# Optimization experiments

Hardware: AMD Instinct MI355X
Metric: run time of the kernel (lower is better)

Reference implementation:

```python
import math
import jax, jax.numpy as jnp
import numpy as np

B, T, D = 2, 1024, 512
H, DK = 8, 64


def setup_inputs() -> dict:
    key = jax.random.key(0)
    ks = jax.random.split(key, 7)
    s = 1.0 / math.sqrt(D)
    x = jax.random.normal(ks[0], (B, T, D), dtype=jnp.float32)
    Wq = jax.random.normal(ks[1], (D, H * DK), dtype=jnp.float32) * s
    Wk = jax.random.normal(ks[2], (D, H * DK), dtype=jnp.float32) * s
    Wv = jax.random.normal(ks[3], (D, H * DK), dtype=jnp.float32) * s
    Wo = jax.random.normal(ks[4], (H * DK, D), dtype=jnp.float32) * s
    Wg = jax.random.normal(ks[5], (D, H * DK), dtype=jnp.float32) * 0.02
    bg = jnp.ones((H * DK,), dtype=jnp.float32)  # gate_bias_init = 1.0
    return {"x": x, "Wq": Wq, "Wk": Wk, "Wv": Wv, "Wo": Wo, "Wg": Wg, "bg": bg}


def reference(x, Wq, Wk, Wv, Wo, Wg, bg):
    b, t, d = x.shape
    Q = jax.nn.relu(x @ Wq).reshape(b, t, H, DK)
    K = jax.nn.relu(x @ Wk).reshape(b, t, H, DK)
    V = (x @ Wv).reshape(b, t, H, DK)
    angle = jnp.arange(t, dtype=x.dtype) * (math.pi / (2 * t))  # (T,)
    cosw = jnp.cos(angle)[None, :, None, None]
    sinw = jnp.sin(angle)[None, :, None, None]
    Qc, Qs = Q * cosw, Q * sinw
    Kc, Ks = K * cosw, K * sinw
    # cumulative KV outer products: (B,T,H,DK,DK)
    Sc = jnp.cumsum(jnp.einsum('bthd,bthe->bthde', Kc, V), axis=1)
    Ss = jnp.cumsum(jnp.einsum('bthd,bthe->bthde', Ks, V), axis=1)
    o = jnp.einsum('bthd,bthde->bthe', Qc, Sc) + jnp.einsum('bthd,bthde->bthe', Qs, Ss)
    zc = jnp.cumsum(Kc, axis=1)
    zs = jnp.cumsum(Ks, axis=1)
    z = jnp.einsum('bthd,bthd->bth', Qc, zc) + jnp.einsum('bthd,bthd->bth', Qs, zs)
    z = jnp.maximum(z, 1e-6)[..., None]
    o = o / z
    gate = jax.nn.sigmoid((x @ Wg + bg).reshape(b, t, H, DK))
    o = o * gate
    return o.reshape(b, t, H * DK) @ Wo
```

## Files before the change

kernel.cpp:

```cpp
#include <hip/hip_runtime.h>
#include <math.h>

#define B_ 2
#define T_ 1024
#define D_ 512
#define H_ 8
#define DK_ 64
#define NBH_ 16
#define C_ 32
#define G_ 32

#define PI_OVER_2T 0.00153398078788564122971808758949f

typedef float f32x4 __attribute__((ext_vector_type(4)));
typedef short s16x8 __attribute__((ext_vector_type(8)));

__device__ __forceinline__ ushort f2bf(float x) {
    unsigned u = __float_as_uint(x);
    unsigned r = (u + 0x7fffu + ((u >> 16) & 1u)) >> 16;
    return (ushort)r;
}
__device__ __forceinline__ float bf2f(ushort u) {
    return __uint_as_float((unsigned)u << 16);
}

__device__ __forceinline__ void async16(void* lds, const void* g) {
    __builtin_amdgcn_global_load_lds(
        (const __attribute__((address_space(1))) void*)g,
        (__attribute__((address_space(3))) void*)lds, 16, 0, 0);
}

__global__ __launch_bounds__(256) void k_conv(
    const float* __restrict__ x,
    const float* __restrict__ Wq, const float* __restrict__ Wk,
    const float* __restrict__ Wv, const float* __restrict__ Wg,
    const float* __restrict__ Wo,
    ushort* __restrict__ xb, ushort* __restrict__ WtAll)
{
    __shared__ float Ts[64][65];
    const int bx = blockIdx.x;
    const int tid = threadIdx.x;
    if (bx < 1024) {
        int i = (bx * 256 + tid) * 4;
        float4 v = *(const float4*)&x[i];
        ushort4 o;
        o.x = f2bf(v.x); o.y = f2bf(v.y); o.z = f2bf(v.z); o.w = f2bf(v.w);
        *(ushort4*)&xb[i] = o;
        return;
    }
    const int bid = bx - 1024;
    const int mi = bid >> 6;
    const int t64 = bid & 63;
    const float* __restrict__ W = (mi == 0) ? Wq : (mi == 1) ? Wk
                                 : (mi == 2) ? Wv : (mi == 3) ? Wg : Wo;
    const int tr = t64 >> 3, tc = t64 & 7;
#pragma unroll
    for (int p = 0; p < 4; p++) {
        int row = p * 16 + (tid >> 4);
        int c4 = (tid & 15) * 4;
        float4 v = *(const float4*)&W[(size_t)(tr * 64 + row) * 512 + tc * 64 + c4];
        Ts[row][c4 + 0] = v.x; Ts[row][c4 + 1] = v.y;
        Ts[row][c4 + 2] = v.z; Ts[row][c4 + 3] = v.w;
    }
    __syncthreads();
    const int nl = tid >> 2, kc = (tid & 3) * 16;
    ushort buf[16];
#pragma unroll
    for (int u = 0; u < 16; u++) buf[u] = f2bf(Ts[kc + u][nl]);
    ushort* dst = WtAll + (size_t)mi * 262144 + (size_t)(tc * 64 + nl) * 512
                  + tr * 64 + kc;
    *(uint4*)dst = *(uint4*)&buf[0];
    *(uint4*)(dst + 8) = *(uint4*)&buf[8];
}

template<int MODE, int TM, int TN>
__global__ __launch_bounds__(256) void k_gemm(
    const ushort* __restrict__ A, const ushort* __restrict__ Bt,
    const float* __restrict__ bg,
    void* __restrict__ O0v, void* __restrict__ O1v,
    void* __restrict__ O2v, void* __restrict__ O3v)
{
    constexpr int WM = TM / 2, WN = TN / 2;
    constexpr int FM = WM / 16, FN = WN / 16;
    constexpr int NA = (TM * 32) / 2048;
    constexpr int NB = (TN * 32) / 2048;

    __shared__ ushort As[2][TM * 32];
    __shared__ ushort Bs[2][TN * 32];

    const int tid = threadIdx.x;
    const int ct = blockIdx.x;
    const int rowBase = blockIdx.y * TM;

    const ushort* __restrict__ Bmat;
    int which = 0, matCol;
    if (MODE == 0) {
        which = ct / (512 / TN);
        matCol = (ct % (512 / TN)) * TN;
        Bmat = Bt + (size_t)which * 262144;
    } else {
        matCol = ct * TN;
        Bmat = Bt;
    }

    const int wave = tid >> 6, lane = tid & 63;
    const int q = lane >> 4, ln = lane & 15;
    const int mB = (wave >> 1) * WM, nB = (wave & 1) * WN;

    int fuA[NA], fuB[NB];
    const ushort* gA[NA];
    const ushort* gB[NB];
#pragma unroll
    for (int u = 0; u < NA; u++) {
        int fu = tid * 8 + u * 2048;
        int r = fu >> 5;
        int c = ((((fu >> 3) & 3) ^ ((r >> 1) & 3))) * 8;
        fuA[u] = fu;
        gA[u] = A + (size_t)(rowBase + r) * 512 + c;
    }
#pragma unroll
    for (int u = 0; u < NB; u++) {
        int fu = tid * 8 + u * 2048;
        int r = fu >> 5;
        int c = ((((fu >> 3) & 3) ^ ((r >> 1) & 3))) * 8;
        fuB[u] = fu;
        gB[u] = Bmat + (size_t)(matCol + r) * 512 + c;
    }

    f32x4 acc[FM][FN];
#pragma unroll
    for (int i = 0; i < FM; i++)
#pragma unroll
        for (int j = 0; j < FN; j++) acc[i][j] = (f32x4){0.f, 0.f, 0.f, 0.f};

    int aoff[FM], boff[FN];
#pragma unroll
    for (int i = 0; i < FM; i++) {
        int ra = mB + i * 16 + ln;
        aoff[i] = ra * 32 + ((q ^ ((ra >> 1) & 3)) * 8);
    }
#pragma unroll
    for (int j = 0; j < FN; j++) {
        int rb = nB + j * 16 + ln;
        boff[j] = rb * 32 + ((q ^ ((rb >> 1) & 3)) * 8);
    }

#pragma unroll
    for (int u = 0; u < NA; u++) async16(&As[0][fuA[u]], gA[u]);
#pragma unroll
    for (int u = 0; u < NB; u++) async16(&Bs[0][fuB[u]], gB[u]);

    int cur = 0;
    for (int kb = 0; kb < 512; kb += 32) {
        __syncthreads();
        if (kb + 32 < 512) {
#pragma unroll
            for (int u = 0; u < NA; u++)
                async16(&As[cur ^ 1][fuA[u]], gA[u] + kb + 32);
#pragma unroll
            for (int u = 0; u < NB; u++)
                async16(&Bs[cur ^ 1][fuB[u]], gB[u] + kb + 32);
        }
        s16x8 af[FM], bf[FN];
#pragma unroll
        for (int i = 0; i < FM; i++) af[i] = *(const s16x8*)&As[cur][aoff[i]];
#pragma unroll
        for (int j = 0; j < FN; j++) bf[j] = *(const s16x8*)&Bs[cur][boff[j]];
#pragma unroll
        for (int i = 0; i < FM; i++)
#pragma unroll
            for (int j = 0; j < FN; j++)
                acc[i][j] = __builtin_amdgcn_mfma_f32_16x16x32_bf16(
                    af[i], bf[j], acc[i][j], 0, 0, 0);
        cur ^= 1;
    }

    if (MODE == 0) {
        ushort* __restrict__ Out = (which == 0) ? (ushort*)O0v
                                  : (which == 1) ? (ushort*)O1v
                                  : (which == 2) ? (ushort*)O2v : (ushort*)O3v;
#pragma unroll
        for (int i = 0; i < FM; i++)
#pragma unroll
            for (int j = 0; j < FN; j++) {
                int col = matCol + nB + j * 16 + ln;
#pragma unroll
                for (int r = 0; r < 4; r++) {
                    int row = rowBase + mB + i * 16 + q * 4 + r;
                    float v = acc[i][j][r];
                    if (which <= 1) v = fmaxf(v, 0.f);
                    else if (which == 3) v = 1.f / (1.f + expf(-(v + bg[col])));
                    Out[(size_t)row * 512 + col] = f2bf(v);
                }
            }
    } else {
        float* __restrict__ Out = (float*)O0v;
#pragma unroll
        for (int i = 0; i < FM; i++)
#pragma unroll
            for (int j = 0; j < FN; j++) {
                int col = matCol + nB + j * 16 + ln;
#pragma unroll
                for (int r = 0; r < 4; r++) {
                    int row = rowBase + mB + i * 16 + q * 4 + r;
                    Out[(size_t)row * 512 + col] = acc[i][j][r];
                }
            }
    }
}

__global__ __launch_bounds__(256) void k_chunk_kv(
    const ushort* __restrict__ Kg, const ushort* __restrict__ Vg,
    ushort* __restrict__ Sst, float* __restrict__ Zst)
{
    __shared__ __align__(16) float Kb[C_ * 64];
    __shared__ __align__(16) float Vb[C_ * 64];
    __shared__ float cosA[C_], sinA[C_];

    const int blk = blockIdx.x;
    const int bh = blk >> 5, g = blk & 31;
    const int b = bh >> 3, h = bh & 7;
    const int tid = threadIdx.x;
    const int rBase = b * T_ + g * C_;
    const int colB = h * DK_;

    {
        int row = tid >> 3, c8 = (tid & 7) * 8;
        size_t ga = (size_t)(rBase + row) * D_ + colB + c8;
        uint4 kraw = *(const uint4*)&Kg[ga];
        uint4 vraw = *(const uint4*)&Vg[ga];
        const ushort* kp = (const ushort*)&kraw;
        const ushort* vp = (const ushort*)&vraw;
#pragma unroll
        for (int u = 0; u < 8; u++) {
            Kb[row * 64 + c8 + u] = bf2f(kp[u]);
            Vb[row * 64 + c8 + u] = bf2f(vp[u]);
        }
    }
    if (tid < C_) {
        float a = (float)(g * C_ + tid) * PI_OVER_2T;
        cosA[tid] = cosf(a); sinA[tid] = sinf(a);
    }
    __syncthreads();

    const int d = tid >> 2;
    const int e0 = (tid & 3) * 16;
    float sc[16], ss[16];
#pragma unroll
    for (int u = 0; u < 16; u++) { sc[u] = 0.f; ss[u] = 0.f; }
    float zc = 0.f, zs = 0.f;

    for (int t = 0; t < C_; t++) {
        float kk = Kb[t * 64 + d];
        float kc = kk * cosA[t], ks = kk * sinA[t];
        zc += kc; zs += ks;
#pragma unroll
        for (int u = 0; u < 4; u++) {
            float4 v4 = *(const float4*)&Vb[t * 64 + e0 + 4 * u];
            sc[4*u+0] += kc * v4.x; sc[4*u+1] += kc * v4.y;
            sc[4*u+2] += kc * v4.z; sc[4*u+3] += kc * v4.w;
            ss[4*u+0] += ks * v4.x; ss[4*u+1] += ks * v4.y;
            ss[4*u+2] += ks * v4.z; ss[4*u+3] += ks * v4.w;
        }
    }

    ushort* Sp = Sst + (size_t)blk * 8192;
    ushort pk[16];
#pragma unroll
    for (int u = 0; u < 16; u++) pk[u] = f2bf(sc[u]);
    *(uint4*)&Sp[d * 64 + e0] = *(uint4*)&pk[0];
    *(uint4*)&Sp[d * 64 + e0 + 8] = *(uint4*)&pk[8];
#pragma unroll
    for (int u = 0; u < 16; u++) pk[u] = f2bf(ss[u]);
    *(uint4*)&Sp[4096 + d * 64 + e0] = *(uint4*)&pk[0];
    *(uint4*)&Sp[4096 + d * 64 + e0 + 8] = *(uint4*)&pk[8];

    if ((tid & 3) == 0) {
        Zst[(size_t)blk * 128 + d] = zc;
        Zst[(size_t)blk * 128 + 64 + d] = zs;
    }
}

__global__ __launch_bounds__(256) void k_scan(
    ushort* __restrict__ Sst, float* __restrict__ Zst)
{
    int id = blockIdx.x * 256 + threadIdx.x;
    if (id < 32768) {
        int bh = id >> 11, i4 = (id & 2047) * 4;
        float4 run = make_float4(0.f, 0.f, 0.f, 0.f);
        for (int g = 0; g < G_; g++) {
            ushort4* a = (ushort4*)&Sst[(size_t)(bh * G_ + g) * 8192 + i4];
            ushort4 t = *a;
            ushort4 o;
            o.x = f2bf(run.x); o.y = f2bf(run.y);
            o.z = f2bf(run.z); o.w = f2bf(run.w);
            *a = o;
            run.x += bf2f(t.x); run.y += bf2f(t.y);
            run.z += bf2f(t.z); run.w += bf2f(t.w);
        }
    } else {
        int id2 = id - 32768;
        if (id2 >= 512) return;
        int bh = id2 >> 5, i4 = (id2 & 31) * 4;
        float4 run = make_float4(0.f, 0.f, 0.f, 0.f);
        for (int g = 0; g < G_; g++) {
            float4* a = (float4*)&Zst[(size_t)(bh * G_ + g) * 128 + i4];
            float4 t = *a;
            *a = run;
            run.x += t.x; run.y += t.y; run.z += t.z; run.w += t.w;
        }
    }
}

__global__ __launch_bounds__(256) void k_out_chunk(
    const ushort* __restrict__ Qg, const ushort* __restrict__ Kg,
    const ushort* __restrict__ Vg, const ushort* __restrict__ Gg,
    const ushort* __restrict__ Sst, const float* __restrict__ Zst,
    ushort* __restrict__ Op)
{
    __shared__ __align__(16) float Qb[C_ * 68];
    __shared__ __align__(16) float R1[64 * 68];
    __shared__ __align__(16) float Scb[64 * 68];
    __shared__ __align__(16) float Ssb[64 * 68];
    __shared__ __align__(16) float Pb[C_ * 36];
    __shared__ float cosA[C_], sinA[C_], zinv[C_], zcb[64], zsb[64];

    const int blk = blockIdx.x;
    const int bh = blk >> 5, g = blk & 31;
    const int b = bh >> 3, h = bh & 7;
    const int tid = threadIdx.x;
    const int rBase = b * T_ + g * C_;
    const int colB = h * DK_;

    {
        int row = tid >> 3, c8 = (tid & 7) * 8;
        size_t ga = (size_t)(rBase + row) * D_ + colB + c8;
        uint4 qraw = *(const uint4*)&Qg[ga];
        uint4 kraw = *(const uint4*)&Kg[ga];
        const ushort* qp = (const ushort*)&qraw;
        const ushort* kp = (const ushort*)&kraw;
#pragma unroll
        for (int u = 0; u < 8; u++) {
            Qb[row * 68 + c8 + u] = bf2f(qp[u]);
            R1[(c8 + u) * 36 + row] = bf2f(kp[u]);
        }
    }
    const ushort* Sbase = Sst + (size_t)blk * 8192;
    for (int v = tid; v < 512; v += 256) {
        int d = v >> 3, e8 = (v & 7) * 8;
        uint4 raw = *(const uint4*)&Sbase[d * 64 + e8];
        const ushort* sp = (const ushort*)&raw;
#pragma unroll
        for (int u = 0; u < 8; u++) Scb[d * 68 + e8 + u] = bf2f(sp[u]);
    }
    for (int v = tid; v < 512; v += 256) {
        int d = v >> 3, e8 = (v & 7) * 8;
        uint4 raw = *(const uint4*)&Sbase[4096 + d * 64 + e8];
        const ushort* sp = (const ushort*)&raw;
#pragma unroll
        for (int u = 0; u < 8; u++) Ssb[d * 68 + e8 + u] = bf2f(sp[u]);
    }
    if (tid < 64) {
        zcb[tid] = Zst[(size_t)blk * 128 + tid];
    } else if (tid < 128) {
        zsb[tid - 64] = Zst[(size_t)blk * 128 + 64 + (tid - 64)];
    } else if (tid < 160) {
        int t = tid - 128;
        float a = (float)(g * C_ + t) * PI_OVER_2T;
        cosA[t] = cosf(a); sinA[t] = sinf(a);
    }
    __syncthreads();

    {
        const int t = tid >> 3;
        const int s4 = (tid & 7) * 4;
        float a0 = 0.f, a1 = 0.f, a2 = 0.f, a3 = 0.f;
#pragma unroll 8
        for (int k = 0; k < 64; k++) {
            float qv = Qb[t * 68 + k];
            float4 kv = *(const float4*)&R1[k * 36 + s4];
            a0 += qv * kv.x; a1 += qv * kv.y; a2 += qv * kv.z; a3 += qv * kv.w;
        }
        float ctt = cosA[t], stt = sinA[t];
        float r[4] = {a0, a1, a2, a3};
        float pr[4];
#pragma unroll
        for (int u = 0; u < 4; u++) {
            int s = s4 + u;
            float w = (s <= t) ? (ctt * cosA[s] + stt * sinA[s]) : 0.f;
            pr[u] = r[u] * w;
        }
        *(float4*)&Pb[t * 36 + s4] = make_float4(pr[0], pr[1], pr[2], pr[3]);
    }
    __syncthreads();

    {
        int row = tid >> 3, c8 = (tid & 7) * 8;
        uint4 vraw = *(const uint4*)&Vg[(size_t)(rBase + row) * D_ + colB + c8];
        const ushort* vp = (const ushort*)&vraw;
#pragma unroll
        for (int u = 0; u < 8; u++) R1[row * 68 + c8 + u] = bf2f(vp[u]);
    }
    if (tid < C_) {
        const int t = tid;
        float ctt = cosA[t], stt = sinA[t];
        float z = 0.f;
        for (int d = 0; d < 64; d++)
            z += Qb[t * 68 + d] * (ctt * zcb[d] + stt * zsb[d]);
        for (int s = 0; s < C_; s++)
            z += Pb[t * 36 + s];
        zinv[t] = 1.f / fmaxf(z, 1e-6f);
    }
    __syncthreads();

    {
        const int t = tid >> 3;
        const int e0 = (tid & 7) * 8;
        float o[8];
#pragma unroll
        for (int u = 0; u < 8; u++) o[u] = 0.f;
        float ctt = cosA[t], stt = sinA[t];
#pragma unroll 4
        for (int d = 0; d < 64; d++) {
            float qv = Qb[t * 68 + d];
            float qc = qv * ctt, qs = qv * stt;
            float4 sc0 = *(const float4*)&Scb[d * 68 + e0];
            float4 sc1 = *(const float4*)&Scb[d * 68 + e0 + 4];
            float4 ss0 = *(const float4*)&Ssb[d * 68 + e0];
            float4 ss1 = *(const float4*)&Ssb[d * 68 + e0 + 4];
            o[0] += qc * sc0.x + qs * ss0.x;
            o[1] += qc * sc0.y + qs * ss0.y;
            o[2] += qc * sc0.z + qs * ss0.z;
            o[3] += qc * sc0.w + qs * ss0.w;
            o[4] += qc * sc1.x + qs * ss1.x;
            o[5] += qc * sc1.y + qs * ss1.y;
            o[6] += qc * sc1.z + qs * ss1.z;
            o[7] += qc * sc1.w + qs * ss1.w;
        }
#pragma unroll 4
        for (int s = 0; s < C_; s++) {
            float p = Pb[t * 36 + s];
            float4 v0 = *(const float4*)&R1[s * 68 + e0];
            float4 v1 = *(const float4*)&R1[s * 68 + e0 + 4];
            o[0] += p * v0.x; o[1] += p * v0.y;
            o[2] += p * v0.z; o[3] += p * v0.w;
            o[4] += p * v1.x; o[5] += p * v1.y;
            o[6] += p * v1.z; o[7] += p * v1.w;
        }
        const float zi = zinv[t];
        size_t go = (size_t)(rBase + t) * D_ + colB + e0;
        uint4 graw = *(const uint4*)&Gg[go];
        const ushort* gp = (const ushort*)&graw;
        ushort r8[8];
#pragma unroll
        for (int u = 0; u < 8; u++) r8[u] = f2bf(o[u] * zi * bf2f(gp[u]));
        *(uint4*)&Op[go] = *(uint4*)r8;
    }
}

extern "C" void kernel_launch(void* const* d_in, const int* in_sizes, int n_in,
                              void* d_out, int out_size, void* d_ws, size_t ws_size,
                              hipStream_t stream)
{
    const float* x  = (const float*)d_in[0];
    const float* Wq = (const float*)d_in[1];
    const float* Wk = (const float*)d_in[2];
    const float* Wv = (const float*)d_in[3];
    const float* Wo = (const float*)d_in[4];
    const float* Wg = (const float*)d_in[5];
    const float* bg = (const float*)d_in[6];
    float* out = (float*)d_out;

    ushort* wsu = (ushort*)d_ws;
    ushort* xb    = wsu;
    ushort* WtAll = xb + 1048576;
    ushort* Qg    = WtAll + 1310720;
    ushort* Kg    = Qg + 1048576;
    ushort* Vg    = Kg + 1048576;
    ushort* Gg    = Vg + 1048576;
    ushort* Sst   = Gg + 1048576;
    ushort* Opb   = Sst + 4194304;
    float*  Zst   = (float*)(Opb + 1048576);

    dim3 blk(256);
    k_conv<<<dim3(1344), blk, 0, stream>>>(x, Wq, Wk, Wv, Wg, Wo, xb, WtAll);
    k_gemm<0, 128, 64><<<dim3(32, 16), blk, 0, stream>>>(
        xb, WtAll, bg, Qg, Kg, Vg, Gg);
    k_chunk_kv<<<dim3(NBH_ * G_), blk, 0, stream>>>(Kg, Vg, Sst, Zst);
    k_scan<<<dim3(130), blk, 0, stream>>>(Sst, Zst);
    k_out_chunk<<<dim3(NBH_ * G_), blk, 0, stream>>>(
        Qg, Kg, Vg, Gg, Sst, Zst, Opb);
    k_gemm<1, 64, 64><<<dim3(8, 32), blk, 0, stream>>>(
        Opb, WtAll + (size_t)4 * 262144, nullptr, out, nullptr, nullptr, nullptr);
}
```

Baseline: 126.8 us.

## Use bf16 MFMA for chunk KV state and intra-chunk attention output

Rewrites the chunk KV-state kernel and the per-chunk output kernel to use 16x16x32 bf16 MFMA instructions in place of scalar fp32 FMA loops. K is pre-scaled by cos/sin and stored transposed in bf16 LDS, and Q is scaled by cos/sin in registers before the MFMA. The change cuts LDS footprint and ALU work. In exchange it adds extra bf16 rounding of intermediates (scaled Q/K, P) and switches to scattered scalar global stores, with the S state now written transposed (e-major).

Measured after the change: 117.7 us. 7.2% less time.

```diff
diff --git a/kernel.cpp b/kernel.cpp
--- a/kernel.cpp
+++ b/kernel.cpp
@@ -22,6 +22,13 @@
 }
 __device__ __forceinline__ float bf2f(ushort u) {
     return __uint_as_float((unsigned)u << 16);
+}
+__device__ __forceinline__ s16x8 bscale(s16x8 v, float s) {
+    s16x8 r;
+#pragma unroll
+    for (int u = 0; u < 8; u++)
+        r[u] = (short)f2bf(bf2f((ushort)v[u]) * s);
+    return r;
 }
 
 __device__ __forceinline__ void async16(void* lds, const void* g) {
@@ -213,9 +220,9 @@
     const ushort* __restrict__ Kg, const ushort* __restrict__ Vg,
     ushort* __restrict__ Sst, float* __restrict__ Zst)
 {
-    __shared__ __align__(16) float Kb[C_ * 64];
-    __shared__ __align__(16) float Vb[C_ * 64];
-    __shared__ float cosA[C_], sinA[C_];
+    __shared__ ushort KcT[64 * 40];
+    __shared__ ushort KsT[64 * 40];
+    __shared__ ushort VT [64 * 40];
 
     const int blk = blockIdx.x;
     const int bh = blk >> 5, g = blk & 31;
@@ -226,6 +233,8 @@
 
     {
         int row = tid >> 3, c8 = (tid & 7) * 8;
+        float a = (float)(g * C_ + row) * PI_OVER_2T;
+        float ca = cosf(a), sa = sinf(a);
         size_t ga = (size_t)(rBase + row) * D_ + colB + c8;
         uint4 kraw = *(const uint4*)&Kg[ga];
         uint4 vraw = *(const uint4*)&Vg[ga];
@@ -233,51 +242,42 @@
         const ushort* vp = (const ushort*)&vraw;
 #pragma unroll
         for (int u = 0; u < 8; u++) {
-            Kb[row * 64 + c8 + u] = bf2f(kp[u]);
-            Vb[row * 64 + c8 + u] = bf2f(vp[u]);
-        }
-    }
-    if (tid < C_) {
-        float a = (float)(g * C_ + tid) * PI_OVER_2T;
-        cosA[tid] = cosf(a); sinA[tid] = sinf(a);
+            float kf = bf2f(kp[u]);
+            KcT[(c8 + u) * 40 + row] = f2bf(kf * ca);
+            KsT[(c8 + u) * 40 + row] = f2bf(kf * sa);
+            VT [(c8 + u) * 40 + row] = vp[u];
+        }
     }
     __syncthreads();
 
-    const int d = tid >> 2;
-    const int e0 = (tid & 3) * 16;
-    float sc[16], ss[16];
-#pragma unroll
-    for (int u = 0; u < 16; u++) { sc[u] = 0.f; ss[u] = 0.f; }
-    float zc = 0.f, zs = 0.f;
-
-    for (int t = 0; t < C_; t++) {
-        float kk = Kb[t * 64 + d];
-        float kc = kk * cosA[t], ks = kk * sinA[t];
-        zc += kc; zs += ks;
-#pragma unroll
-        for (int u = 0; u < 4; u++) {
-            float4 v4 = *(const float4*)&Vb[t * 64 + e0 + 4 * u];
-            sc[4*u+0] += kc * v4.x; sc[4*u+1] += kc * v4.y;
-            sc[4*u+2] += kc * v4.z; sc[4*u+3] += kc * v4.w;
-            ss[4*u+0] += ks * v4.x; ss[4*u+1] += ks * v4.y;
-            ss[4*u+2] += ks * v4.z; ss[4*u+3] += ks * v4.w;
-        }
-    }
-
+    if (tid < 128) {
+        int d = tid & 63;
+        const ushort* src = (tid < 64) ? KcT : KsT;
+        float zsum = 0.f;
+#pragma unroll
+        for (int t = 0; t < C_; t++) zsum += bf2f(src[d * 40 + t]);
+        Zst[(size_t)blk * 128 + tid] = zsum;
+    }
+
+    const int wave = tid >> 6, lane = tid & 63;
+    const int q = lane >> 4, ln = lane & 15;
+    s16x8 av = *(const s16x8*)&VT[(wave * 16 + ln) * 40 + q * 8];
     ushort* Sp = Sst + (size_t)blk * 8192;
-    ushort pk[16];
-#pragma unroll
-    for (int u = 0; u < 16; u++) pk[u] = f2bf(sc[u]);
-    *(uint4*)&Sp[d * 64 + e0] = *(uint4*)&pk[0];
-    *(uint4*)&Sp[d * 64 + e0 + 8] = *(uint4*)&pk[8];
-#pragma unroll
-    for (int u = 0; u < 16; u++) pk[u] = f2bf(ss[u]);
-    *(uint4*)&Sp[4096 + d * 64 + e0] = *(uint4*)&pk[0];
-    *(uint4*)&Sp[4096 + d * 64 + e0 + 8] = *(uint4*)&pk[8];
-
-    if ((tid & 3) == 0) {
-        Zst[(size_t)blk * 128 + d] = zc;
-        Zst[(size_t)blk * 128 + 64 + d] = zs;
+#pragma unroll
+    for (int nj = 0; nj < 4; nj++) {
+        s16x8 bc = *(const s16x8*)&KcT[(nj * 16 + ln) * 40 + q * 8];
+        s16x8 bs = *(const s16x8*)&KsT[(nj * 16 + ln) * 40 + q * 8];
+        f32x4 ac = __builtin_amdgcn_mfma_f32_16x16x32_bf16(
+            av, bc, (f32x4){0.f, 0.f, 0.f, 0.f}, 0, 0, 0);
+        f32x4 as = __builtin_amdgcn_mfma_f32_16x16x32_bf16(
+            av, bs, (f32x4){0.f, 0.f, 0.f, 0.f}, 0, 0, 0);
+#pragma unroll
+        for (int r = 0; r < 4; r++) {
+            int e = wave * 16 + q * 4 + r;
+            int d = nj * 16 + ln;
+            Sp[e * 64 + d] = f2bf(ac[r]);
+            Sp[4096 + e * 64 + d] = f2bf(as[r]);
+        }
     }
 }
 
@@ -318,12 +318,9 @@
     const ushort* __restrict__ Sst, const float* __restrict__ Zst,
     ushort* __restrict__ Op)
 {
-    __shared__ __align__(16) float Qb[C_ * 68];
-    __shared__ __align__(16) float R1[64 * 68];
-    __shared__ __align__(16) float Scb[64 * 68];
-    __shared__ __align__(16) float Ssb[64 * 68];
-    __shared__ __align__(16) float Pb[C_ * 36];
-    __shared__ float cosA[C_], sinA[C_], zinv[C_], zcb[64], zsb[64];
+    __shared__ ushort VT[64 * 40];
+    __shared__ ushort Pb[32 * 40];
+    __shared__ float zinv[32];
 
     const int blk = blockIdx.x;
     const int bh = blk >> 5, g = blk & 31;
@@ -331,130 +328,106 @@
     const int tid = threadIdx.x;
     const int rBase = b * T_ + g * C_;
     const int colB = h * DK_;
-
-    {
-        int row = tid >> 3, c8 = (tid & 7) * 8;
-        size_t ga = (size_t)(rBase + row) * D_ + colB + c8;
-        uint4 qraw = *(const uint4*)&Qg[ga];
-        uint4 kraw = *(const uint4*)&Kg[ga];
-        const ushort* qp = (const ushort*)&qraw;
-        const ushort* kp = (const ushort*)&kraw;
-#pragma unroll
-        for (int u = 0; u < 8; u++) {
-            Qb[row * 68 + c8 + u] = bf2f(qp[u]);
-            R1[(c8 + u) * 36 + row] = bf2f(kp[u]);
-        }
-    }
-    const ushort* Sbase = Sst + (size_t)blk * 8192;
-    for (int v = tid; v < 512; v += 256) {
-        int d = v >> 3, e8 = (v & 7) * 8;
-        uint4 raw = *(const uint4*)&Sbase[d * 64 + e8];
-        const ushort* sp = (const ushort*)&raw;
-#pragma unroll
-        for (int u = 0; u < 8; u++) Scb[d * 68 + e8 + u] = bf2f(sp[u]);
-    }
-    for (int v = tid; v < 512; v += 256) {
-        int d = v >> 3, e8 = (v & 7) * 8;
-        uint4 raw = *(const uint4*)&Sbase[4096 + d * 64 + e8];
-        const ushort* sp = (const ushort*)&raw;
-#pragma unroll
-        for (int u = 0; u < 8; u++) Ssb[d * 68 + e8 + u] = bf2f(sp[u]);
-    }
-    if (tid < 64) {
-        zcb[tid] = Zst[(size_t)blk * 128 + tid];
-    } else if (tid < 128) {
-        zsb[tid - 64] = Zst[(size_t)blk * 128 + 64 + (tid - 64)];
-    } else if (tid < 160) {
-        int t = tid - 128;
-        float a = (float)(g * C_ + t) * PI_OVER_2T;
-        cosA[t] = cosf(a); sinA[t] = sinf(a);
-    }
-    __syncthreads();
-
-    {
-        const int t = tid >> 3;
-        const int s4 = (tid & 7) * 4;
-        float a0 = 0.f, a1 = 0.f, a2 = 0.f, a3 = 0.f;
-#pragma unroll 8
-        for (int k = 0; k < 64; k++) {
-            float qv = Qb[t * 68 + k];
-            float4 kv = *(const float4*)&R1[k * 36 + s4];
-            a0 += qv * kv.x; a1 += qv * kv.y; a2 += qv * kv.z; a3 += qv * kv.w;
-        }
-        float ctt = cosA[t], stt = sinA[t];
-        float r[4] = {a0, a1, a2, a3};
-        float pr[4];
-#pragma unroll
-        for (int u = 0; u < 4; u++) {
-            int s = s4 + u;
-            float w = (s <= t) ? (ctt * cosA[s] + stt * sinA[s]) : 0.f;
-            pr[u] = r[u] * w;
-        }
-        *(float4*)&Pb[t * 36 + s4] = make_float4(pr[0], pr[1], pr[2], pr[3]);
-    }
-    __syncthreads();
+    const int wave = tid >> 6, lane = tid & 63;
+    const int q = lane >> 4, ln = lane & 15;
 
     {
         int row = tid >> 3, c8 = (tid & 7) * 8;
         uint4 vraw = *(const uint4*)&Vg[(size_t)(rBase + row) * D_ + colB + c8];
         const ushort* vp = (const ushort*)&vraw;
 #pragma unroll
-        for (int u = 0; u < 8; u++) R1[row * 68 + c8 + u] = bf2f(vp[u]);
-    }
-    if (tid < C_) {
-        const int t = tid;
-        float ctt = cosA[t], stt = sinA[t];
-        float z = 0.f;
-        for (int d = 0; d < 64; d++)
-            z += Qb[t * 68 + d] * (ctt * zcb[d] + stt * zsb[d]);
-        for (int s = 0; s < C_; s++)
-            z += Pb[t * 36 + s];
-        zinv[t] = 1.f / fmaxf(z, 1e-6f);
+        for (int u = 0; u < 8; u++) VT[(c8 + u) * 40 + row] = vp[u];
+    }
+
+    const int mi = wave >> 1, njp = wave & 1;
+    const ushort* qrow = Qg + (size_t)(rBase + mi * 16 + ln) * D_ + colB;
+    s16x8 aq0 = *(const s16x8*)&qrow[q * 8];
+    s16x8 aq1 = *(const s16x8*)&qrow[32 + q * 8];
+    {
+        const ushort* krow = Kg + (size_t)(rBase + njp * 16 + ln) * D_ + colB;
+        s16x8 bk0 = *(const s16x8*)&krow[q * 8];
+        s16x8 bk1 = *(const s16x8*)&krow[32 + q * 8];
+        f32x4 pacc = __builtin_amdgcn_mfma_f32_16x16x32_bf16(
+            aq0, bk0, (f32x4){0.f, 0.f, 0.f, 0.f}, 0, 0, 0);
+        pacc = __builtin_amdgcn_mfma_f32_16x16x32_bf16(aq1, bk1, pacc, 0, 0, 0);
+        int sl = njp * 16 + ln;
+        float as_ = (float)(g * C_ + sl) * PI_OVER_2T;
+        float cs_ = cosf(as_), ss_ = sinf(as_);
+#pragma unroll
+        for (int r = 0; r < 4; r++) {
+            int tl = mi * 16 + q * 4 + r;
+            float at = (float)(g * C_ + tl) * PI_OVER_2T;
+            float w = (sl <= tl) ? (cosf(at) * cs_ + sinf(at) * ss_) : 0.f;
+            Pb[tl * 40 + sl] = f2bf(pacc[r] * w);
+        }
     }
     __syncthreads();
 
     {
-        const int t = tid >> 3;
-        const int e0 = (tid & 7) * 8;
-        float o[8];
-#pragma unroll
-        for (int u = 0; u < 8; u++) o[u] = 0.f;
-        float ctt = cosA[t], stt = sinA[t];
-#pragma unroll 4
-        for (int d = 0; d < 64; d++) {
-            float qv = Qb[t * 68 + d];
-            float qc = qv * ctt, qs = qv * stt;
-            float4 sc0 = *(const float4*)&Scb[d * 68 + e0];
-            float4 sc1 = *(const float4*)&Scb[d * 68 + e0 + 4];
-            float4 ss0 = *(const float4*)&Ssb[d * 68 + e0];
-            float4 ss1 = *(const float4*)&Ssb[d * 68 + e0 + 4];
-            o[0] += qc * sc0.x + qs * ss0.x;
-            o[1] += qc * sc0.y + qs * ss0.y;
-            o[2] += qc * sc0.z + qs * ss0.z;
-            o[3] += qc * sc0.w + qs * ss0.w;
-            o[4] += qc * sc1.x + qs * ss1.x;
-            o[5] += qc * sc1.y + qs * ss1.y;
-            o[6] += qc * sc1.z + qs * ss1.z;
-            o[7] += qc * sc1.w + qs * ss1.w;
-        }
-#pragma unroll 4
-        for (int s = 0; s < C_; s++) {
-            float p = Pb[t * 36 + s];
-            float4 v0 = *(const float4*)&R1[s * 68 + e0];
-            float4 v1 = *(const float4*)&R1[s * 68 + e0 + 4];
-            o[0] += p * v0.x; o[1] += p * v0.y;
-            o[2] += p * v0.z; o[3] += p * v0.w;
-            o[4] += p * v1.x; o[5] += p * v1.y;
-            o[6] += p * v1.z; o[7] += p * v1.w;
-        }
-        const float zi = zinv[t];
-        size_t go = (size_t)(rBase + t) * D_ + colB + e0;
-        uint4 graw = *(const uint4*)&Gg[go];
-        const ushort* gp = (const ushort*)&graw;
-        ushort r8[8];
-#pragma unroll
-        for (int u = 0; u < 8; u++) r8[u] = f2bf(o[u] * zi * bf2f(gp[u]));
-        *(uint4*)&Op[go] = *(uint4*)r8;
+        int t = tid >> 3, sub = tid & 7;
+        uint4 qraw = *(const uint4*)&Qg[(size_t)(rBase + t) * D_ + colB + sub * 8];
+        const ushort* qp = (const ushort*)&qraw;
+        const float* zcp = Zst + (size_t)blk * 128 + sub * 8;
+        float4 zc0 = *(const float4*)&zcp[0];
+        float4 zc1 = *(const float4*)&zcp[4];
+        float4 zs0 = *(const float4*)&zcp[64];
+        float4 zs1 = *(const float4*)&zcp[68];
+        float pc = 0.f, ps = 0.f;
+        float zcv[8] = {zc0.x, zc0.y, zc0.z, zc0.w, zc1.x, zc1.y, zc1.z, zc1.w};
+        float zsv[8] = {zs0.x, zs0.y, zs0.z, zs0.w, zs1.x, zs1.y, zs1.z, zs1.w};
+#pragma unroll
+        for (int u = 0; u < 8; u++) {
+            float qf = bf2f(qp[u]);
+            pc += qf * zcv[u]; ps += qf * zsv[u];
+        }
+        float pr = 0.f;
+#pragma unroll
+        for (int u = 0; u < 4; u++) pr += bf2f(Pb[t * 40 + sub * 4 + u]);
+#pragma unroll
+        for (int m = 1; m < 8; m <<= 1) {
+            pc += __shfl_xor(pc, m);
+            ps += __shfl_xor(ps, m);
+            pr += __shfl_xor(pr, m);
+        }
+        if (sub == 0) {
+            float at = (float)(g * C_ + t) * PI_OVER_2T;
+            float z = cosf(at) * pc + sinf(at) * ps + pr;
+            zinv[t] = 1.f / fmaxf(z, 1e-6f);
+        }
+    }
+    __syncthreads();
+
+    {
+        float am = (float)(g * C_ + mi * 16 + ln) * PI_OVER_2T;
+        float cm = cosf(am), sm = sinf(am);
+        s16x8 aqc0 = bscale(aq0, cm), aqc1 = bscale(aq1, cm);
+        s16x8 aqs0 = bscale(aq0, sm), aqs1 = bscale(aq1, sm);
+        s16x8 pf = *(const s16x8*)&Pb[(mi * 16 + ln) * 40 + q * 8];
+        const ushort* Sp = Sst + (size_t)blk * 8192;
+#pragma unroll
+        for (int jj = 0; jj < 2; jj++) {
+            int nj = 2 * (wave & 1) + jj;
+            const ushort* scp = Sp + (nj * 16 + ln) * 64;
+            s16x8 bc0 = *(const s16x8*)&scp[q * 8];
+            s16x8 bc1 = *(const s16x8*)&scp[32 + q * 8];
+            s16x8 bs0 = *(const s16x8*)&scp[4096 + q * 8];
+            s16x8 bs1 = *(const s16x8*)&scp[4096 + 32 + q * 8];
+            s16x8 bv  = *(const s16x8*)&VT[(nj * 16 + ln) * 40 + q * 8];
+            f32x4 acc = __builtin_amdgcn_mfma_f32_16x16x32_bf16(
+                pf, bv, (f32x4){0.f, 0.f, 0.f, 0.f}, 0, 0, 0);
+            acc = __builtin_amdgcn_mfma_f32_16x16x32_bf16(aqc0, bc0, acc, 0, 0, 0);
+            acc = __builtin_amdgcn_mfma_f32_16x16x32_bf16(aqc1, bc1, acc, 0, 0, 0);
+            acc = __builtin_amdgcn_mfma_f32_16x16x32_bf16(aqs0, bs0, acc, 0, 0, 0);
+            acc = __builtin_amdgcn_mfma_f32_16x16x32_bf16(aqs1, bs1, acc, 0, 0, 0);
+#pragma unroll
+            for (int r = 0; r < 4; r++) {
+                int tl = mi * 16 + q * 4 + r;
+                int e = nj * 16 + ln;
+                size_t go = (size_t)(rBase + tl) * D_ + colB + e;
+                float o = acc[r] * zinv[tl] * bf2f(Gg[go]);
+                Op[go] = f2bf(o);
+            }
+        }
     }
 }
 
```
